# Optimization experiments

Hardware: AMD Instinct MI355X
Metric: run time of the kernel (lower is better)

The kernel has to match this reference:

```python
import jax, jax.numpy as jnp
import numpy as np

N, C, DK, DV = 8192, 128, 64, 64


def setup_inputs() -> dict:
    key = jax.random.key(0)
    ks = jax.random.split(key, 7)
    x = jax.random.normal(ks[0], (N, C), dtype=jnp.float32)
    # kaiming_normal for weights (std = sqrt(2/fan_in)), torch-default uniform bias
    std = float(np.sqrt(2.0 / C))
    bb = float(1.0 / np.sqrt(C))
    Wq = jax.random.normal(ks[1], (DK, C), dtype=jnp.float32) * std
    Wk = jax.random.normal(ks[2], (DK, C), dtype=jnp.float32) * std
    Wv = jax.random.normal(ks[3], (DV, C), dtype=jnp.float32) * std
    bq = jax.random.uniform(ks[4], (DK,), dtype=jnp.float32, minval=-bb, maxval=bb)
    bk = jax.random.uniform(ks[5], (DK,), dtype=jnp.float32, minval=-bb, maxval=bb)
    bv = jax.random.uniform(ks[6], (DV,), dtype=jnp.float32, minval=-bb, maxval=bb)
    return {"polyline_feature": x, "Wq": Wq, "bq": bq, "Wk": Wk, "bk": bk, "Wv": Wv, "bv": bv}


def reference(polyline_feature, Wq, bq, Wk, bk, Wv, bv):
    x = polyline_feature
    Q = jax.nn.relu(x @ Wq.T + bq)  # [N, DK]
    K = jax.nn.relu(x @ Wk.T + bk)  # [N, DK]
    V = jax.nn.relu(x @ Wv.T + bv)  # [N, DV]
    scores = (Q @ K.T) / jnp.sqrt(jnp.asarray(K.shape[1], Q.dtype))  # [N, N]
    attn = jax.nn.softmax(scores, axis=1)
    return attn @ V + Q  # residual on Q (non-standard)
```

## Files before the change

kernel.cpp:

```cpp
#include <hip/hip_runtime.h>


typedef __attribute__((ext_vector_type(8))) __bf16 bf16x8;
typedef __attribute__((ext_vector_type(4))) float f32x4;
typedef __attribute__((ext_vector_type(16))) float f32x16;

constexpr int N_ROWS = 8192;
constexpr int CDIM   = 128;
constexpr int DKV    = 64;
constexpr float SCALE_Q = 0.125f * 1.4426950408889634f;

__device__ __forceinline__ float fast_exp2(float x) {
    return __builtin_amdgcn_exp2f(x);
}

__device__ __forceinline__ unsigned short f2bf(float x) {
    union { float f; unsigned u; } v; v.f = x;
    unsigned r = v.u + 0x7fffu + ((v.u >> 16) & 1u);
    return (unsigned short)(r >> 16);
}

__device__ __forceinline__ float bf2f(unsigned short h) {
    union { unsigned u; float f; } v; v.u = (unsigned)h << 16; return v.f;
}

union Frag {
    unsigned u32[4];
    unsigned short u16[8];
    bf16x8 b;
    f32x4 f;
};

__global__ __launch_bounds__(128) void qkv_kernel(
    const float* __restrict__ x,
    const float* __restrict__ Wq, const float* __restrict__ bq,
    const float* __restrict__ Wk, const float* __restrict__ bk,
    const float* __restrict__ Wv, const float* __restrict__ bv,
    unsigned short* __restrict__ Qb, unsigned short* __restrict__ Kb,
    unsigned short* __restrict__ Vt, float* __restrict__ Qf)
{
    const int tid = threadIdx.x;
    const int w  = tid >> 6;
    const int l  = tid & 63;
    const int g  = l >> 4;
    const int lm = l & 15;
    const int n_base = blockIdx.x * 32 + w * 16;

    bf16x8 af[4];
    {
        const float* xrow = x + (size_t)(n_base + lm) * CDIM;
        #pragma unroll
        for (int s = 0; s < 4; ++s) {
            f32x4 lo = *(const f32x4*)(xrow + s * 32 + g * 8);
            f32x4 hi = *(const f32x4*)(xrow + s * 32 + g * 8 + 4);
            Frag fr;
            #pragma unroll
            for (int j = 0; j < 4; ++j) { fr.u16[j] = f2bf(lo[j]); fr.u16[4 + j] = f2bf(hi[j]); }
            af[s] = fr.b;
        }
    }

    const float* Ws[3] = {Wq, Wk, Wv};
    const float* Bs[3] = {bq, bk, bv};
    #pragma unroll
    for (int mat = 0; mat < 3; ++mat) {
        #pragma unroll
        for (int ct = 0; ct < 4; ++ct) {
            const int f = ct * 16 + lm;
            const float* wrow = Ws[mat] + (size_t)f * CDIM;
            f32x4 acc = {0.f, 0.f, 0.f, 0.f};
            #pragma unroll
            for (int s = 0; s < 4; ++s) {
                f32x4 lo = *(const f32x4*)(wrow + s * 32 + g * 8);
                f32x4 hi = *(const f32x4*)(wrow + s * 32 + g * 8 + 4);
                Frag fr;
                #pragma unroll
                for (int j = 0; j < 4; ++j) { fr.u16[j] = f2bf(lo[j]); fr.u16[4 + j] = f2bf(hi[j]); }
                acc = __builtin_amdgcn_mfma_f32_16x16x32_bf16(af[s], fr.b, acc, 0, 0, 0);
            }
            const float bias = Bs[mat][f];
            #pragma unroll
            for (int j = 0; j < 4; ++j) {
                const int n = n_base + g * 4 + j;
                const float v = fmaxf(acc[j] + bias, 0.f);
                if (mat == 0) {
                    Qf[(size_t)n * DKV + f] = v;
                    Qb[(size_t)n * DKV + f] = f2bf(v * SCALE_Q);
                } else if (mat == 1) {
                    Kb[(size_t)n * DKV + f] = f2bf(v);
                } else {
                    Vt[(size_t)f * N_ROWS + n] = f2bf(v);
                }
            }
        }
    }
}

__global__ __launch_bounds__(512, 4) void attn_kernel(
    const unsigned short* __restrict__ Qb, const unsigned short* __restrict__ Kb,
    const unsigned short* __restrict__ Vt,
    unsigned short* __restrict__ PartOb, float* __restrict__ PartL,
    int kv_per_split)
{
    __shared__ __align__(16) unsigned short K_lds[2][64 * 64];
    __shared__ __align__(16) unsigned short V_lds[2][64 * 64];

    const int tid = threadIdx.x;
    const int w  = tid >> 6;
    const int l  = tid & 63;
    const int c  = l & 31;
    const int hB = l >> 5;
    const int qb = blockIdx.x;
    const int sp = blockIdx.y;
    const int q0 = qb * 256 + w * 32;
    const int kv0 = sp * kv_per_split;

    const int r_ = w * 8 + (l >> 3);
    const int perm_ = (r_ & 7) ^ (((r_ >> 3) & 3) << 1);
    const int srcc = ((l & 7) ^ perm_) * 8;

#define ISSUE_LOADS(T, B) do { \
    const int kvt_ = kv0 + (T) * 64; \
    __builtin_amdgcn_global_load_lds( \
        (const __attribute__((address_space(1))) unsigned int*)(Kb + (size_t)(kvt_ + r_) * DKV + srcc), \
        (__attribute__((address_space(3))) unsigned int*)&K_lds[B][w * 8 * 64], 16, 0, 0); \
    __builtin_amdgcn_global_load_lds( \
        (const __attribute__((address_space(1))) unsigned int*)(Vt + (size_t)r_ * N_ROWS + kvt_ + srcc), \
        (__attribute__((address_space(3))) unsigned int*)&V_lds[B][w * 8 * 64], 16, 0, 0); \
} while (0)

    bf16x8 qf0, qf1, qf2, qf3;
    {
        const unsigned short* qp = Qb + (size_t)(q0 + c) * DKV + hB * 8;
        qf0 = *(const bf16x8*)(qp);
        qf1 = *(const bf16x8*)(qp + 16);
        qf2 = *(const bf16x8*)(qp + 32);
        qf3 = *(const bf16x8*)(qp + 48);
    }

    f32x16 o0 = {}, o1 = {};
    float lsum = 0.f;

    const int nt = kv_per_split >> 6;
    ISSUE_LOADS(0, 0);
    if (nt > 1) ISSUE_LOADS(1, 1);
    __syncthreads();

    const int swz = ((c & 7) ^ (((c >> 3) & 3) << 1)) << 4;

    for (int t = 0; t < nt; ++t) {
        const char* Kl = (const char*)&K_lds[t & 1][0];
        const char* Vl = (const char*)&V_lds[t & 1][0];

        f32x16 st0 = {}, st1 = {};
        #pragma unroll
        for (int ks = 0; ks < 4; ++ks) {
            const int cb = ks * 32 + hB * 16;
            bf16x8 a0 = *(const bf16x8*)(Kl + c * 128 + (cb ^ swz));
            bf16x8 a1 = *(const bf16x8*)(Kl + (32 + c) * 128 + (cb ^ swz));
            const bf16x8 qv = (ks == 0) ? qf0 : (ks == 1) ? qf1 : (ks == 2) ? qf2 : qf3;
            st0 = __builtin_amdgcn_mfma_f32_32x32x16_bf16(a0, qv, st0, 0, 0, 0);
            st1 = __builtin_amdgcn_mfma_f32_32x32x16_bf16(a1, qv, st1, 0, 0, 0);
        }

        unsigned pk[16];
        float ls = 0.f;
        #pragma unroll
        for (int p = 0; p < 8; ++p) {
            float a = fast_exp2(st0[2 * p]);
            float b = fast_exp2(st0[2 * p + 1]);
            ls += a + b;
            union { unsigned u; __bf16 h[2]; } uu;
            uu.h[0] = (__bf16)a; uu.h[1] = (__bf16)b;
            pk[p] = uu.u;
        }
        #pragma unroll
        for (int p = 0; p < 8; ++p) {
            float a = fast_exp2(st1[2 * p]);
            float b = fast_exp2(st1[2 * p + 1]);
            ls += a + b;
            union { unsigned u; __bf16 h[2]; } uu;
            uu.h[0] = (__bf16)a; uu.h[1] = (__bf16)b;
            pk[8 + p] = uu.u;
        }
        lsum += ls;

        #pragma unroll
        for (int ks = 0; ks < 4; ++ks) {
            const int base = (ks >> 1) * 8 + (ks & 1) * 4;
            const unsigned ownA  = hB ? pk[base + 2] : pk[base + 0];
            const unsigned ownB  = hB ? pk[base + 3] : pk[base + 1];
            const unsigned contA = hB ? pk[base + 0] : pk[base + 2];
            const unsigned contB = hB ? pk[base + 1] : pk[base + 3];
            const unsigned crossA = __shfl_xor(contA, 32);
            const unsigned crossB = __shfl_xor(contB, 32);
            Frag pf;
            pf.u32[0] = hB ? crossA : ownA;
            pf.u32[1] = hB ? crossB : ownB;
            pf.u32[2] = hB ? ownA : crossA;
            pf.u32[3] = hB ? ownB : crossB;
            const int cb = ks * 32 + hB * 16;
            bf16x8 v0 = *(const bf16x8*)(Vl + c * 128 + (cb ^ swz));
            bf16x8 v1 = *(const bf16x8*)(Vl + (32 + c) * 128 + (cb ^ swz));
            o0 = __builtin_amdgcn_mfma_f32_32x32x16_bf16(v0, pf.b, o0, 0, 0, 0);
            o1 = __builtin_amdgcn_mfma_f32_32x32x16_bf16(v1, pf.b, o1, 0, 0, 0);
        }

        __syncthreads();
        if (t + 2 < nt) ISSUE_LOADS(t + 2, t & 1);
    }
#undef ISSUE_LOADS

    lsum += __shfl_xor(lsum, 32);

    {
        unsigned short* po = PartOb + ((size_t)sp * N_ROWS + q0 + c) * 64;
        #pragma unroll
        for (int rq = 0; rq < 4; ++rq) {
            union { unsigned u[2]; __bf16 h[4]; } pa, pb;
            #pragma unroll
            for (int j = 0; j < 4; ++j) { pa.h[j] = (__bf16)o0[4 * rq + j]; pb.h[j] = (__bf16)o1[4 * rq + j]; }
            *(uint2*)(po + 8 * rq + 4 * hB)      = *(uint2*)pa.u;
            *(uint2*)(po + 32 + 8 * rq + 4 * hB) = *(uint2*)pb.u;
        }
    }
    if (hB == 0)
        PartL[(size_t)sp * N_ROWS + q0 + c] = lsum;
}

__global__ __launch_bounds__(256) void merge_kernel(
    const unsigned short* __restrict__ PartOb, const float* __restrict__ PartL,
    const float* __restrict__ Qf, float* __restrict__ out, int split)
{
    const int gid = blockIdx.x * 256 + threadIdx.x;
    const int q  = gid >> 5;
    const int dp = gid & 31;

    float L = 0.f, a0 = 0.f, a1 = 0.f;
    for (int s = 0; s < split; ++s) {
        L += PartL[(size_t)s * N_ROWS + q];
        const unsigned v = *(const unsigned*)(PartOb + ((size_t)s * N_ROWS + q) * 64 + 2 * dp);
        a0 += bf2f((unsigned short)(v & 0xffffu));
        a1 += bf2f((unsigned short)(v >> 16));
    }
    const float invL = 1.f / L;
    const int d0 = 2 * dp;
    out[(size_t)q * 64 + d0]     = a0 * invL + Qf[(size_t)q * 64 + d0];
    out[(size_t)q * 64 + d0 + 1] = a1 * invL + Qf[(size_t)q * 64 + d0 + 1];
}

extern "C" void kernel_launch(void* const* d_in, const int* in_sizes, int n_in,
                              void* d_out, int out_size, void* d_ws, size_t ws_size,
                              hipStream_t stream)
{
    const float* x  = (const float*)d_in[0];
    const float* Wq = (const float*)d_in[1];
    const float* bq = (const float*)d_in[2];
    const float* Wk = (const float*)d_in[3];
    const float* bk = (const float*)d_in[4];
    const float* Wv = (const float*)d_in[5];
    const float* bv = (const float*)d_in[6];
    float* out = (float*)d_out;

    char* ws = (char*)d_ws;
    size_t off = 0;
    auto take = [&](size_t bytes) {
        char* p = ws + off;
        off += (bytes + 255) & ~(size_t)255;
        return p;
    };
    unsigned short* Qb = (unsigned short*)take((size_t)N_ROWS * DKV * 2);
    unsigned short* Kb = (unsigned short*)take((size_t)N_ROWS * DKV * 2);
    unsigned short* Vt = (unsigned short*)take((size_t)DKV * N_ROWS * 2);
    float*          Qf = (float*)take((size_t)N_ROWS * DKV * 4);

    int split = 16;
    const size_t per_split = (size_t)N_ROWS * 64 * 2 + (size_t)N_ROWS * 4 + 512;
    while (split > 1 && off + (size_t)split * per_split > ws_size) split >>= 1;

    unsigned short* PartOb = (unsigned short*)take((size_t)split * N_ROWS * 64 * 2);
    float*          PartL  = (float*)take((size_t)split * N_ROWS * 4);

    qkv_kernel<<<dim3(N_ROWS / 32), dim3(128), 0, stream>>>(
        x, Wq, bq, Wk, bk, Wv, bv, Qb, Kb, Vt, Qf);
    attn_kernel<<<dim3(N_ROWS / 256, split), dim3(512), 0, stream>>>(
        Qb, Kb, Vt, PartOb, PartL, N_ROWS / split);
    merge_kernel<<<dim3(N_ROWS * 32 / 256), dim3(256), 0, stream>>>(
        PartOb, PartL, Qf, out, split);
}
```

Before: 49.39 us.

## Load whole 256-key KV chunk per block and split across 32 partitions

The attention kernel stops double-buffering 64-key tiles in a loop. Each block now loads one 256-key chunk of K and V into LDS in a single pass, using a new swizzle for V, with one barrier before compute. Split-K doubles to 32 so each block handles exactly one chunk, which removes the per-tile barriers and raises the block count. In exchange there is no overlap of loads with compute inside a block, more partial outputs for the merge kernel to read, and LDS use per block doubles to 64 KB, which may cut occupancy.

```diff
diff --git a/kernel.cpp b/kernel.cpp
--- a/kernel.cpp
+++ b/kernel.cpp
@@ -8,6 +8,7 @@
 constexpr int N_ROWS = 8192;
 constexpr int CDIM   = 128;
 constexpr int DKV    = 64;
+constexpr int KVS    = 256;
 constexpr float SCALE_Q = 0.125f * 1.4426950408889634f;
 
 __device__ __forceinline__ float fast_exp2(float x) {
@@ -100,10 +101,10 @@
     const unsigned short* __restrict__ Qb, const unsigned short* __restrict__ Kb,
     const unsigned short* __restrict__ Vt,
     unsigned short* __restrict__ PartOb, float* __restrict__ PartL,
-    int kv_per_split)
-{
-    __shared__ __align__(16) unsigned short K_lds[2][64 * 64];
-    __shared__ __align__(16) unsigned short V_lds[2][64 * 64];
+    int nchunk)
+{
+    __shared__ __align__(16) unsigned short K_lds[KVS * DKV];
+    __shared__ __align__(16) unsigned short V_lds[DKV * KVS];
 
     const int tid = threadIdx.x;
     const int w  = tid >> 6;
@@ -113,21 +114,6 @@
     const int qb = blockIdx.x;
     const int sp = blockIdx.y;
     const int q0 = qb * 256 + w * 32;
-    const int kv0 = sp * kv_per_split;
-
-    const int r_ = w * 8 + (l >> 3);
-    const int perm_ = (r_ & 7) ^ (((r_ >> 3) & 3) << 1);
-    const int srcc = ((l & 7) ^ perm_) * 8;
-
-#define ISSUE_LOADS(T, B) do { \
-    const int kvt_ = kv0 + (T) * 64; \
-    __builtin_amdgcn_global_load_lds( \
-        (const __attribute__((address_space(1))) unsigned int*)(Kb + (size_t)(kvt_ + r_) * DKV + srcc), \
-        (__attribute__((address_space(3))) unsigned int*)&K_lds[B][w * 8 * 64], 16, 0, 0); \
-    __builtin_amdgcn_global_load_lds( \
-        (const __attribute__((address_space(1))) unsigned int*)(Vt + (size_t)r_ * N_ROWS + kvt_ + srcc), \
-        (__attribute__((address_space(3))) unsigned int*)&V_lds[B][w * 8 * 64], 16, 0, 0); \
-} while (0)
 
     bf16x8 qf0, qf1, qf2, qf3;
     {
@@ -141,75 +127,86 @@
     f32x16 o0 = {}, o1 = {};
     float lsum = 0.f;
 
-    const int nt = kv_per_split >> 6;
-    ISSUE_LOADS(0, 0);
-    if (nt > 1) ISSUE_LOADS(1, 1);
-    __syncthreads();
-
-    const int swz = ((c & 7) ^ (((c >> 3) & 3) << 1)) << 4;
-
-    for (int t = 0; t < nt; ++t) {
-        const char* Kl = (const char*)&K_lds[t & 1][0];
-        const char* Vl = (const char*)&V_lds[t & 1][0];
-
-        f32x16 st0 = {}, st1 = {};
-        #pragma unroll
-        for (int ks = 0; ks < 4; ++ks) {
-            const int cb = ks * 32 + hB * 16;
-            bf16x8 a0 = *(const bf16x8*)(Kl + c * 128 + (cb ^ swz));
-            bf16x8 a1 = *(const bf16x8*)(Kl + (32 + c) * 128 + (cb ^ swz));
-            const bf16x8 qv = (ks == 0) ? qf0 : (ks == 1) ? qf1 : (ks == 2) ? qf2 : qf3;
-            st0 = __builtin_amdgcn_mfma_f32_32x32x16_bf16(a0, qv, st0, 0, 0, 0);
-            st1 = __builtin_amdgcn_mfma_f32_32x32x16_bf16(a1, qv, st1, 0, 0, 0);
-        }
-
-        unsigned pk[16];
-        float ls = 0.f;
-        #pragma unroll
-        for (int p = 0; p < 8; ++p) {
-            float a = fast_exp2(st0[2 * p]);
-            float b = fast_exp2(st0[2 * p + 1]);
-            ls += a + b;
-            union { unsigned u; __bf16 h[2]; } uu;
-            uu.h[0] = (__bf16)a; uu.h[1] = (__bf16)b;
-            pk[p] = uu.u;
-        }
-        #pragma unroll
-        for (int p = 0; p < 8; ++p) {
-            float a = fast_exp2(st1[2 * p]);
-            float b = fast_exp2(st1[2 * p + 1]);
-            ls += a + b;
-            union { unsigned u; __bf16 h[2]; } uu;
-            uu.h[0] = (__bf16)a; uu.h[1] = (__bf16)b;
-            pk[8 + p] = uu.u;
-        }
-        lsum += ls;
-
-        #pragma unroll
-        for (int ks = 0; ks < 4; ++ks) {
-            const int base = (ks >> 1) * 8 + (ks & 1) * 4;
-            const unsigned ownA  = hB ? pk[base + 2] : pk[base + 0];
-            const unsigned ownB  = hB ? pk[base + 3] : pk[base + 1];
-            const unsigned contA = hB ? pk[base + 0] : pk[base + 2];
-            const unsigned contB = hB ? pk[base + 1] : pk[base + 3];
-            const unsigned crossA = __shfl_xor(contA, 32);
-            const unsigned crossB = __shfl_xor(contB, 32);
-            Frag pf;
-            pf.u32[0] = hB ? crossA : ownA;
-            pf.u32[1] = hB ? crossB : ownB;
-            pf.u32[2] = hB ? ownA : crossA;
-            pf.u32[3] = hB ? ownB : crossB;
-            const int cb = ks * 32 + hB * 16;
-            bf16x8 v0 = *(const bf16x8*)(Vl + c * 128 + (cb ^ swz));
-            bf16x8 v1 = *(const bf16x8*)(Vl + (32 + c) * 128 + (cb ^ swz));
-            o0 = __builtin_amdgcn_mfma_f32_32x32x16_bf16(v0, pf.b, o0, 0, 0, 0);
-            o1 = __builtin_amdgcn_mfma_f32_32x32x16_bf16(v1, pf.b, o1, 0, 0, 0);
-        }
-
+    const int swzK = ((c & 7) ^ (((c >> 3) & 3) << 1)) << 4;
+
+    for (int ch = 0; ch < nchunk; ++ch) {
+        const int kv0 = (sp * nchunk + ch) * KVS;
+        if (ch > 0) __syncthreads();
+
+        #pragma unroll
+        for (int i = 0; i < 4; ++i) {
+            const int rk = w * 8 + (l >> 3) + 64 * i;
+            const int sk = ((l & 7) ^ ((rk & 7) ^ (((rk >> 3) & 3) << 1))) * 8;
+            __builtin_amdgcn_global_load_lds(
+                (const __attribute__((address_space(1))) unsigned int*)(Kb + (size_t)(kv0 + rk) * DKV + sk),
+                (__attribute__((address_space(3))) unsigned int*)&K_lds[i * 4096 + w * 512], 16, 0, 0);
+            const int rv = w * 2 + (l >> 5) + 16 * i;
+            const int sv = ((l & 31) ^ (rv & 31)) * 8;
+            __builtin_amdgcn_global_load_lds(
+                (const __attribute__((address_space(1))) unsigned int*)(Vt + (size_t)rv * N_ROWS + kv0 + sv),
+                (__attribute__((address_space(3))) unsigned int*)&V_lds[i * 4096 + w * 512], 16, 0, 0);
+        }
         __syncthreads();
-        if (t + 2 < nt) ISSUE_LOADS(t + 2, t & 1);
-    }
-#undef ISSUE_LOADS
+
+        #pragma unroll
+        for (int kt = 0; kt < 4; ++kt) {
+            const char* Kl = (const char*)K_lds + (size_t)kt * 64 * 128;
+
+            f32x16 st0 = {}, st1 = {};
+            #pragma unroll
+            for (int ks = 0; ks < 4; ++ks) {
+                const int cb = ks * 32 + hB * 16;
+                bf16x8 a0 = *(const bf16x8*)(Kl + c * 128 + (cb ^ swzK));
+                bf16x8 a1 = *(const bf16x8*)(Kl + (32 + c) * 128 + (cb ^ swzK));
+                const bf16x8 qv = (ks == 0) ? qf0 : (ks == 1) ? qf1 : (ks == 2) ? qf2 : qf3;
+                st0 = __builtin_amdgcn_mfma_f32_32x32x16_bf16(a0, qv, st0, 0, 0, 0);
+                st1 = __builtin_amdgcn_mfma_f32_32x32x16_bf16(a1, qv, st1, 0, 0, 0);
+            }
+
+            unsigned pk[16];
+            float ls = 0.f;
+            #pragma unroll
+            for (int p = 0; p < 8; ++p) {
+                float a = fast_exp2(st0[2 * p]);
+                float b = fast_exp2(st0[2 * p + 1]);
+                ls += a + b;
+                union { unsigned u; __bf16 h[2]; } uu;
+                uu.h[0] = (__bf16)a; uu.h[1] = (__bf16)b;
+                pk[p] = uu.u;
+            }
+            #pragma unroll
+            for (int p = 0; p < 8; ++p) {
+                float a = fast_exp2(st1[2 * p]);
+                float b = fast_exp2(st1[2 * p + 1]);
+                ls += a + b;
+                union { unsigned u; __bf16 h[2]; } uu;
+                uu.h[0] = (__bf16)a; uu.h[1] = (__bf16)b;
+                pk[8 + p] = uu.u;
+            }
+            lsum += ls;
+
+            #pragma unroll
+            for (int ks = 0; ks < 4; ++ks) {
+                const int base = (ks >> 1) * 8 + (ks & 1) * 4;
+                const unsigned ownA  = hB ? pk[base + 2] : pk[base + 0];
+                const unsigned ownB  = hB ? pk[base + 3] : pk[base + 1];
+                const unsigned contA = hB ? pk[base + 0] : pk[base + 2];
+                const unsigned contB = hB ? pk[base + 1] : pk[base + 3];
+                const unsigned crossA = __shfl_xor(contA, 32);
+                const unsigned crossB = __shfl_xor(contB, 32);
+                Frag pf;
+                pf.u32[0] = hB ? crossA : ownA;
+                pf.u32[1] = hB ? crossB : ownB;
+                pf.u32[2] = hB ? ownA : crossA;
+                pf.u32[3] = hB ? ownB : crossB;
+                const int sl = (kt * 8 + ks * 2 + hB) ^ c;
+                bf16x8 v0 = *(const bf16x8*)((const char*)V_lds + c * 512 + sl * 16);
+                bf16x8 v1 = *(const bf16x8*)((const char*)V_lds + (32 + c) * 512 + sl * 16);
+                o0 = __builtin_amdgcn_mfma_f32_32x32x16_bf16(v0, pf.b, o0, 0, 0, 0);
+                o1 = __builtin_amdgcn_mfma_f32_32x32x16_bf16(v1, pf.b, o1, 0, 0, 0);
+            }
+        }
+    }
 
     lsum += __shfl_xor(lsum, 32);
 
@@ -274,9 +271,9 @@
     unsigned short* Vt = (unsigned short*)take((size_t)DKV * N_ROWS * 2);
     float*          Qf = (float*)take((size_t)N_ROWS * DKV * 4);
 
-    int split = 16;
+    int split = 32, nchunk = 1;
     const size_t per_split = (size_t)N_ROWS * 64 * 2 + (size_t)N_ROWS * 4 + 512;
-    while (split > 1 && off + (size_t)split * per_split > ws_size) split >>= 1;
+    while (split > 1 && off + (size_t)split * per_split > ws_size) { split >>= 1; nchunk <<= 1; }
 
     unsigned short* PartOb = (unsigned short*)take((size_t)split * N_ROWS * 64 * 2);
     float*          PartL  = (float*)take((size_t)split * N_ROWS * 4);
@@ -284,7 +281,7 @@
     qkv_kernel<<<dim3(N_ROWS / 32), dim3(128), 0, stream>>>(
         x, Wq, bq, Wk, bk, Wv, bv, Qb, Kb, Vt, Qf);
     attn_kernel<<<dim3(N_ROWS / 256, split), dim3(512), 0, stream>>>(
-        Qb, Kb, Vt, PartOb, PartL, N_ROWS / split);
+        Qb, Kb, Vt, PartOb, PartL, nchunk);
     merge_kernel<<<dim3(N_ROWS * 32 / 256), dim3(256), 0, stream>>>(
         PartOb, PartL, Qf, out, split);
 }
```

Result: slower. 139.4 us (+182.3%).
